# Optimization experiments

Hardware: AMD Instinct MI355X
Metric: run time of the kernel (lower is better)

The kernel has to match this reference:

```python
import jax, jax.numpy as jnp
import numpy as np

B, C, H, W = 8, 256, 64, 64
EPS = 1e-5


def _mk_conv_bn(key, oc, ic):
    k = jax.random.split(key, 6)
    return dict(
        w=jax.random.normal(k[0], (oc, ic), jnp.float32) * 0.01,  # trunc-normal approx, stddev 0.01
        b=jnp.zeros((oc,), jnp.float32),
        s=jax.random.uniform(k[1], (oc,), jnp.float32, 0.5, 1.5),   # BN scale
        t=jax.random.normal(k[2], (oc,), jnp.float32) * 0.1,        # BN shift
        m=jax.random.normal(k[3], (oc,), jnp.float32) * 0.1,        # BN running mean
        v=jax.random.uniform(k[4], (oc,), jnp.float32, 0.5, 1.5),   # BN running var
    )


def setup_inputs() -> dict:
    key = jax.random.key(0)
    ks = jax.random.split(key, 6)
    d = {"x": jax.random.normal(ks[0], (B, C, H, W), jnp.float32)}
    for i, (oc, ic) in zip([1, 2, 3, 4], [(C // 8, C), (C // 8, C), (C // 2, C), (C, C // 2)]):
        p = _mk_conv_bn(ks[i], oc, ic)
        for name, val in p.items():
            d[f"{name}{i}"] = val
    d["gamma"] = jnp.asarray(0.5, jnp.float32)
    return d


def _cbn(x, w, b, s, t, m, v, relu=True):
    # conv1x1 + BatchNorm(eval) [+ ReLU]; dropout is identity at inference
    y = jnp.einsum('bchw,oc->bohw', x, w) + b[None, :, None, None]
    scale = (s / jnp.sqrt(v + EPS))[None, :, None, None]
    y = (y - m[None, :, None, None]) * scale + t[None, :, None, None]
    return jax.nn.relu(y) if relu else y


def _maxpool2(x):
    b, c, h, w = x.shape
    return x.reshape(b, c, h // 2, 2, w // 2, 2).max(axis=(3, 5))


def reference(x, w1, b1, s1, t1, m1, v1, w2, b2, s2, t2, m2, v2,
              w3, b3, s3, t3, m3, v3, w4, b4, s4, t4, m4, v4, gamma):
    b, c, h, w = x.shape
    f = _maxpool2(_cbn(x, w1, b1, s1, t1, m1, v1))   # (B, C/8, H/2, W/2)
    g = _cbn(x, w2, b2, s2, t2, m2, v2)              # (B, C/8, H, W)
    hh = _maxpool2(_cbn(x, w3, b3, s3, t3, m3, v3))  # (B, C/2, H/2, W/2)
    hw, hw4 = h * w, (h // 2) * (w // 2)
    f = f.reshape(b, c // 8, hw4).transpose(0, 2, 1)  # (B, HW/4, C/8)
    g = g.reshape(b, c // 8, hw)                      # (B, C/8, HW)
    s = jnp.einsum('bnk,bkm->bnm', f, g)              # (B, HW/4, HW)
    beta = jax.nn.softmax(s, axis=1)                  # softmax over dim=1, as in source
    hh = hh.reshape(b, c // 2, hw4)                   # (B, C/2, HW/4)
    o = jnp.einsum('bcn,bnm->bcm', hh, beta).reshape(b, c // 2, h, w)
    out = _cbn(o, w4, b4, s4, t4, m4, v4, relu=False)
    return gamma * out + x
```

## Files before the change

kernel.cpp:

```cpp
#include <hip/hip_runtime.h>
#include <hip/hip_bf16.h>

#define HW   4096
#define HW4  1024
#define EPS  1e-5f
#define SM_SHIFT 20.0f

typedef __attribute__((ext_vector_type(8))) short bf16x8;
typedef __attribute__((ext_vector_type(4))) float f32x4;

__device__ __forceinline__ short f2bs(float f) {
    union { float f; unsigned u; } v; v.f = f;
    unsigned r = v.u + 0x7FFFu + ((v.u >> 16) & 1u);
    return (short)(r >> 16);
}
__device__ __forceinline__ float bs2f(short s) {
    union { unsigned u; float f; } v; v.u = ((unsigned)(unsigned short)s) << 16;
    return v.f;
}
__device__ __forceinline__ int swz64(int r, int c)  { return (r << 6) + ((c ^ (r & 7))  << 3); }
__device__ __forceinline__ int swz128(int r, int c) { return (r << 7) + ((c ^ (r & 15)) << 3); }
__device__ __forceinline__ int p40(int r, int c)    { return r * 40 + c * 8; }

__global__ __launch_bounds__(256) void conv123pool(
    const float* __restrict__ x,
    const float* __restrict__ w1, const float* __restrict__ b1, const float* __restrict__ s1,
    const float* __restrict__ t1, const float* __restrict__ m1, const float* __restrict__ v1,
    const float* __restrict__ w2, const float* __restrict__ b2, const float* __restrict__ s2,
    const float* __restrict__ t2, const float* __restrict__ m2, const float* __restrict__ v2,
    const float* __restrict__ w3, const float* __restrict__ b3, const float* __restrict__ s3,
    const float* __restrict__ t3, const float* __restrict__ m3, const float* __restrict__ v3,
    short* __restrict__ gbuf, short* __restrict__ fbuf, short* __restrict__ hhbuf)
{
    __shared__ __align__(16) short Wl[96 * 64];
    __shared__ __align__(16) short Xl[128 * 64];
    __shared__ float alB[96], beB[96];

    const int t = threadIdx.x;
    const int lane = t & 63, wv = t >> 6;
    const int quad = lane >> 4, l16 = lane & 15;
    const int ptile = blockIdx.x;
    const int ocg   = blockIdx.y;
    const int bz    = blockIdx.z;
    const int pBase = ptile * 128;
    const int wcol  = (wv & 1) * 32;
    const int woch  = (wv >> 1) * 48;

    if (t < 96) {
        int j = ocg * 96 + t;
        float pb, ps, ptv, pm, pv;
        if (j < 32)      { pb = b1[j]; ps = s1[j]; ptv = t1[j]; pm = m1[j]; pv = v1[j]; }
        else if (j < 64) { int c = j - 32; pb = b2[c]; ps = s2[c]; ptv = t2[c]; pm = m2[c]; pv = v2[c]; }
        else             { int c = j - 64; pb = b3[c]; ps = s3[c]; ptv = t3[c]; pm = m3[c]; pv = v3[c]; }
        float al = ps * rsqrtf(pv + EPS);
        alB[t] = al; beB[t] = (pb - pm) * al + ptv;
    }

    const f32x4 fzero = {0.f, 0.f, 0.f, 0.f};
    f32x4 acc[3][4];
    #pragma unroll
    for (int i = 0; i < 3; ++i)
        #pragma unroll
        for (int j = 0; j < 4; ++j) acc[i][j] = fzero;

    const int ptOff0 = wcol, ptOff1 = wcol + 16, ptOff2 = wcol + 64, ptOff3 = wcol + 80;
    const int xp  = t & 127, xk8 = t >> 7;

    for (int k0 = 0; k0 < 256; k0 += 64) {
        #pragma unroll
        for (int i = 0; i < 2; ++i) {
            int idx = t + i * 256;
            if (i == 0 || t < 128) {
                int oc = idx >> 2, kb = (idx & 3) * 16;
                int j = ocg * 96 + oc;
                const float* wp = (j < 32) ? (w1 + j * 256)
                                : (j < 64) ? (w2 + (j - 32) * 256)
                                           : (w3 + (j - 64) * 256);
                wp += k0 + kb;
                float4 a = *(const float4*)(wp);
                float4 b = *(const float4*)(wp + 4);
                float4 c = *(const float4*)(wp + 8);
                float4 d = *(const float4*)(wp + 12);
                bf16x8 lo, hi;
                lo[0]=f2bs(a.x); lo[1]=f2bs(a.y); lo[2]=f2bs(a.z); lo[3]=f2bs(a.w);
                lo[4]=f2bs(b.x); lo[5]=f2bs(b.y); lo[6]=f2bs(b.z); lo[7]=f2bs(b.w);
                hi[0]=f2bs(c.x); hi[1]=f2bs(c.y); hi[2]=f2bs(c.z); hi[3]=f2bs(c.w);
                hi[4]=f2bs(d.x); hi[5]=f2bs(d.y); hi[6]=f2bs(d.z); hi[7]=f2bs(d.w);
                *(bf16x8*)&Wl[swz64(oc, (kb >> 3))]     = lo;
                *(bf16x8*)&Wl[swz64(oc, (kb >> 3) + 1)] = hi;
            }
        }
        {
            const float* xp0 = x + ((size_t)bz * 256 + k0 + xk8 * 32) * HW + pBase + xp;
            float fv[32];
            #pragma unroll
            for (int i = 0; i < 32; ++i) fv[i] = xp0[(size_t)i * HW];
            #pragma unroll
            for (int c = 0; c < 4; ++c) {
                bf16x8 v;
                #pragma unroll
                for (int jj = 0; jj < 8; ++jj) v[jj] = f2bs(fv[c * 8 + jj]);
                *(bf16x8*)&Xl[swz64(xp, xk8 * 4 + c)] = v;
            }
        }
        __syncthreads();
        #pragma unroll
        for (int kk = 0; kk < 2; ++kk) {
            bf16x8 bfr[4];
            bfr[0] = *(const bf16x8*)&Xl[swz64(ptOff0 + l16, kk * 4 + quad)];
            bfr[1] = *(const bf16x8*)&Xl[swz64(ptOff1 + l16, kk * 4 + quad)];
            bfr[2] = *(const bf16x8*)&Xl[swz64(ptOff2 + l16, kk * 4 + quad)];
            bfr[3] = *(const bf16x8*)&Xl[swz64(ptOff3 + l16, kk * 4 + quad)];
            #pragma unroll
            for (int tt = 0; tt < 3; ++tt) {
                bf16x8 afr = *(const bf16x8*)&Wl[swz64(woch + tt * 16 + l16, kk * 4 + quad)];
                #pragma unroll
                for (int pt = 0; pt < 4; ++pt)
                    acc[tt][pt] = __builtin_amdgcn_mfma_f32_16x16x32_bf16(afr, bfr[pt], acc[tt][pt], 0, 0, 0);
            }
        }
        __syncthreads();
    }

    #pragma unroll
    for (int tt = 0; tt < 3; ++tt) {
        #pragma unroll
        for (int r = 0; r < 4; ++r) {
            int ocl = woch + tt * 16 + quad * 4 + r;
            int j = ocg * 96 + ocl;
            float al = alB[ocl], be = beB[ocl];
            float y[4];
            y[0] = fmaxf(acc[tt][0][r] * al + be, 0.f);
            y[1] = fmaxf(acc[tt][1][r] * al + be, 0.f);
            y[2] = fmaxf(acc[tt][2][r] * al + be, 0.f);
            y[3] = fmaxf(acc[tt][3][r] * al + be, 0.f);
            if (j >= 32 && j < 64) {
                size_t base = ((size_t)bz * 32 + (j - 32)) * HW + pBase;
                gbuf[base + ptOff0 + l16] = f2bs(y[0]);
                gbuf[base + ptOff1 + l16] = f2bs(y[1]);
                gbuf[base + ptOff2 + l16] = f2bs(y[2]);
                gbuf[base + ptOff3 + l16] = f2bs(y[3]);
            } else {
                #pragma unroll
                for (int c = 0; c < 2; ++c) {
                    float v  = fmaxf(y[c], y[c + 2]);
                    float po = fmaxf(v, __shfl_xor(v, 1));
                    if ((l16 & 1) == 0) {
                        int col = wcol + c * 16 + l16;
                        int n = ptile * 32 + (col >> 1);
                        if (j < 32) fbuf[((size_t)bz * 32 + j) * HW4 + n] = f2bs(po);
                        else        hhbuf[((size_t)bz * 128 + (j - 64)) * HW4 + n] = f2bs(po);
                    }
                }
            }
        }
    }
}

__global__ __launch_bounds__(256, 5) void attn_partial(
    const short* __restrict__ gbuf,
    const short* __restrict__ fbuf,
    const short* __restrict__ hhbuf,
    short* __restrict__ opart,
    float* __restrict__ Zbuf)
{
    __shared__ __align__(16) short smem[13312];
    short* gTl = smem;
    short* fTl = smem + 2560;
    short* sTl = smem + 5120;
    short* hhl = smem + 9216;

    const int t = threadIdx.x;
    const int lane = t & 63, wv = t >> 6;
    const int quad = lane >> 4, l16 = lane & 15;
    const int bz = blockIdx.z;
    const int np = blockIdx.y & 1;
    const int cp = blockIdx.y >> 1;
    const int m0 = blockIdx.x * 64;
    const int ms = wv * 16;
    const f32x4 fzero = {0.f, 0.f, 0.f, 0.f};

    {
        int mm = t & 63, k8 = t >> 6;
        bf16x8 v;
        #pragma unroll
        for (int j = 0; j < 8; ++j)
            v[j] = gbuf[((size_t)bz * 32 + k8 * 8 + j) * HW + m0 + mm];
        *(bf16x8*)&gTl[p40(mm, k8)] = v;
    }
    __syncthreads();
    bf16x8 bg = *(const bf16x8*)&gTl[p40(ms + l16, quad)];

    const int fnn = t & 63, fk8 = t >> 6;
    const int hrow = t >> 3, hnc = t & 7;
    const short* fB = fbuf + (size_t)bz * 32 * HW4;
    const short* hB = hhbuf + ((size_t)bz * 128 + cp * 64) * HW4;

    float psum = 0.f;
    f32x4 oacc[4];
    #pragma unroll
    for (int i = 0; i < 4; ++i) oacc[i] = fzero;

    const int nbase = np * 512;
    for (int n0 = nbase; n0 < nbase + 512; n0 += 64) {
        __syncthreads();
        {
            bf16x8 v;
            #pragma unroll
            for (int j = 0; j < 8; ++j)
                v[j] = fB[(fk8 * 8 + j) * HW4 + n0 + fnn];
            *(bf16x8*)&fTl[p40(fnn, fk8)] = v;
        }
        {
            #pragma unroll
            for (int i = 0; i < 2; ++i)
                *(bf16x8*)&hhl[swz64(i * 32 + hrow, hnc)] =
                    *(const bf16x8*)(hB + (size_t)(i * 32 + hrow) * HW4 + n0 + hnc * 8);
        }
        __syncthreads();

        f32x4 sacc[4];
        #pragma unroll
        for (int nt = 0; nt < 4; ++nt) {
            bf16x8 af = *(const bf16x8*)&fTl[p40(nt * 16 + l16, quad)];
            sacc[nt] = __builtin_amdgcn_mfma_f32_16x16x32_bf16(af, bg, fzero, 0, 0, 0);
        }

        #pragma unroll
        for (int nt = 0; nt < 4; ++nt) {
            short4 ev;
            #pragma unroll
            for (int r = 0; r < 4; ++r) {
                float e = __expf(sacc[nt][r] - SM_SHIFT);
                psum += e;
                ((short*)&ev)[r] = f2bs(e);
            }
            int chunk = nt * 2 + (quad >> 1);
            *(short4*)&sTl[swz64(ms + l16, chunk) + (quad & 1) * 4] = ev;
        }

        #pragma unroll
        for (int kk = 0; kk < 2; ++kk) {
            bf16x8 bs = *(const bf16x8*)&sTl[swz64(ms + l16, kk * 4 + quad)];
            #pragma unroll
            for (int ct = 0; ct < 4; ++ct) {
                bf16x8 ah = *(const bf16x8*)&hhl[swz64(ct * 16 + l16, kk * 4 + quad)];
                oacc[ct] = __builtin_amdgcn_mfma_f32_16x16x32_bf16(ah, bs, oacc[ct], 0, 0, 0);
            }
        }
    }

    psum += __shfl_xor(psum, 16);
    psum += __shfl_xor(psum, 32);
    int m = m0 + ms + l16;
    if (cp == 0 && quad == 0)
        Zbuf[((size_t)bz * 2 + np) * HW + m] = psum;

    #pragma unroll
    for (int ct = 0; ct < 4; ++ct) {
        short4 ov;
        #pragma unroll
        for (int r = 0; r < 4; ++r) ((short*)&ov)[r] = f2bs(oacc[ct][r]);
        *(short4*)(opart + (((size_t)bz * 2 + np) * HW + m) * 128 + cp * 64 + ct * 16 + quad * 4) = ov;
    }
}

__global__ __launch_bounds__(256) void conv4_merge(
    const short* __restrict__ opart,
    const float* __restrict__ Zbuf,
    const float* __restrict__ x,
    const float* __restrict__ w4, const float* __restrict__ b4, const float* __restrict__ s4,
    const float* __restrict__ t4, const float* __restrict__ m4, const float* __restrict__ v4,
    const float* __restrict__ gamma, float* __restrict__ out)
{
    __shared__ __align__(16) short smem[24576];
    __shared__ float alB4[256], beB4[256];
    short* o_l = smem;
    short* Wl4 = smem + 8192;

    const int t = threadIdx.x;
    const int lane = t & 63, wv = t >> 6;
    const int quad = lane >> 4, l16 = lane & 15;
    const int bz = blockIdx.y;
    const int m0 = blockIdx.x * 64;
    const f32x4 fzero = {0.f, 0.f, 0.f, 0.f};

    {
        float al = s4[t] * rsqrtf(v4[t] + EPS);
        alB4[t] = al; beB4[t] = (b4[t] - m4[t]) * al + t4[t];
    }

    {
        int m = t >> 2, cb = (t & 3) * 32;
        size_t mi = (size_t)m0 + m;
        const short* p0 = opart + (((size_t)bz * 2 + 0) * HW + mi) * 128 + cb;
        const short* p1 = opart + (((size_t)bz * 2 + 1) * HW + mi) * 128 + cb;
        float z = Zbuf[((size_t)bz * 2 + 0) * HW + mi] + Zbuf[((size_t)bz * 2 + 1) * HW + mi];
        float inv = 1.0f / z;
        #pragma unroll
        for (int seg = 0; seg < 4; ++seg) {
            bf16x8 a = *(const bf16x8*)(p0 + seg * 8);
            bf16x8 b = *(const bf16x8*)(p1 + seg * 8);
            bf16x8 o;
            #pragma unroll
            for (int j = 0; j < 8; ++j)
                o[j] = f2bs((bs2f(a[j]) + bs2f(b[j])) * inv);
            *(bf16x8*)&o_l[swz128(m, (cb >> 3) + seg)] = o;
        }
    }

    f32x4 acc4[4][4];
    #pragma unroll
    for (int i = 0; i < 4; ++i)
        #pragma unroll
        for (int j = 0; j < 4; ++j) acc4[i][j] = fzero;

    for (int c0 = 0; c0 < 128; c0 += 64) {
        #pragma unroll
        for (int i = 0; i < 4; ++i) {
            int oc = i * 64 + (t >> 2);
            int kb = (t & 3) * 16;
            const float* wp = w4 + oc * 128 + c0 + kb;
            float4 a = *(const float4*)(wp);
            float4 b = *(const float4*)(wp + 4);
            float4 c = *(const float4*)(wp + 8);
            float4 d = *(const float4*)(wp + 12);
            bf16x8 lo, hi;
            lo[0]=f2bs(a.x); lo[1]=f2bs(a.y); lo[2]=f2bs(a.z); lo[3]=f2bs(a.w);
            lo[4]=f2bs(b.x); lo[5]=f2bs(b.y); lo[6]=f2bs(b.z); lo[7]=f2bs(b.w);
            hi[0]=f2bs(c.x); hi[1]=f2bs(c.y); hi[2]=f2bs(c.z); hi[3]=f2bs(c.w);
            hi[4]=f2bs(d.x); hi[5]=f2bs(d.y); hi[6]=f2bs(d.z); hi[7]=f2bs(d.w);
            *(bf16x8*)&Wl4[swz64(oc, (kb >> 3))]     = lo;
            *(bf16x8*)&Wl4[swz64(oc, (kb >> 3) + 1)] = hi;
        }
        __syncthreads();
        #pragma unroll
        for (int kk = 0; kk < 2; ++kk) {
            bf16x8 bfr[4];
            #pragma unroll
            for (int mt = 0; mt < 4; ++mt)
                bfr[mt] = *(const bf16x8*)&o_l[swz128(mt * 16 + l16, (c0 >> 3) + kk * 4 + quad)];
            #pragma unroll
            for (int ot = 0; ot < 4; ++ot) {
                bf16x8 afr = *(const bf16x8*)&Wl4[swz64(wv * 64 + ot * 16 + l16, kk * 4 + quad)];
                #pragma unroll
                for (int mt = 0; mt < 4; ++mt)
                    acc4[ot][mt] = __builtin_amdgcn_mfma_f32_16x16x32_bf16(afr, bfr[mt], acc4[ot][mt], 0, 0, 0);
            }
        }
        __syncthreads();
    }

    float gm = gamma[0];
    #pragma unroll
    for (int ot = 0; ot < 4; ++ot) {
        #pragma unroll
        for (int r = 0; r < 4; ++r) {
            int oc = wv * 64 + ot * 16 + quad * 4 + r;
            float al = alB4[oc], be = beB4[oc];
            #pragma unroll
            for (int mt = 0; mt < 4; ++mt) {
                int p = m0 + mt * 16 + l16;
                float y  = acc4[ot][mt][r] * al + be;
                float xo = x[((size_t)bz * 256 + oc) * HW + p];
                out[((size_t)bz * 256 + oc) * HW + p] = gm * y + xo;
            }
        }
    }
}

extern "C" void kernel_launch(void* const* d_in, const int* in_sizes, int n_in,
                              void* d_out, int out_size, void* d_ws, size_t ws_size,
                              hipStream_t stream)
{
    const float* x  = (const float*)d_in[0];
    const float* w1 = (const float*)d_in[1];
    const float* b1 = (const float*)d_in[2];
    const float* s1 = (const float*)d_in[3];
    const float* t1 = (const float*)d_in[4];
    const float* m1 = (const float*)d_in[5];
    const float* v1 = (const float*)d_in[6];
    const float* w2 = (const float*)d_in[7];
    const float* b2 = (const float*)d_in[8];
    const float* s2 = (const float*)d_in[9];
    const float* t2 = (const float*)d_in[10];
    const float* m2 = (const float*)d_in[11];
    const float* v2 = (const float*)d_in[12];
    const float* w3 = (const float*)d_in[13];
    const float* b3 = (const float*)d_in[14];
    const float* s3 = (const float*)d_in[15];
    const float* t3 = (const float*)d_in[16];
    const float* m3 = (const float*)d_in[17];
    const float* v3 = (const float*)d_in[18];
    const float* w4 = (const float*)d_in[19];
    const float* b4 = (const float*)d_in[20];
    const float* s4 = (const float*)d_in[21];
    const float* t4 = (const float*)d_in[22];
    const float* m4 = (const float*)d_in[23];
    const float* v4 = (const float*)d_in[24];
    const float* gm = (const float*)d_in[25];
    float* out = (float*)d_out;

    short* gbuf  = (short*)d_ws;
    short* fbuf  = gbuf  + (size_t)8 * 32 * 4096;
    short* hhbuf = fbuf  + (size_t)8 * 32 * 1024;
    short* opart = hhbuf + (size_t)8 * 128 * 1024;
    float* Zbuf  = (float*)(opart + (size_t)8 * 2 * 4096 * 128);

    conv123pool<<<dim3(32, 2, 8), 256, 0, stream>>>(
        x, w1, b1, s1, t1, m1, v1, w2, b2, s2, t2, m2, v2, w3, b3, s3, t3, m3, v3,
        gbuf, fbuf, hhbuf);
    attn_partial<<<dim3(64, 4, 8), 256, 0, stream>>>(
        gbuf, fbuf, hhbuf, opart, Zbuf);
    conv4_merge<<<dim3(64, 8), 256, 0, stream>>>(
        opart, Zbuf, x, w4, b4, s4, t4, m4, v4, gm, out);
}
```

Baseline: 179.3 us.

## Fuse attention and conv4 into one kernel, dropping split-N partials

Merges the attention-partial kernel and the conv4 merge kernel into a single kernel. Each block now covers all 1024 keys and all 128 hh channels and normalizes by its own softmax sum. It then runs the conv4 GEMM directly from shared memory, so the bf16 opart and Zbuf round trip through global memory and one launch go away. The trade-off is far less parallelism: 512 blocks instead of 2048, and each block does a longer serial loop with more accumulators, which may lower occupancy and latency hiding.

```diff
diff --git a/kernel.cpp b/kernel.cpp
--- a/kernel.cpp
+++ b/kernel.cpp
@@ -13,10 +13,6 @@
     union { float f; unsigned u; } v; v.f = f;
     unsigned r = v.u + 0x7FFFu + ((v.u >> 16) & 1u);
     return (short)(r >> 16);
-}
-__device__ __forceinline__ float bs2f(short s) {
-    union { unsigned u; float f; } v; v.u = ((unsigned)(unsigned short)s) << 16;
-    return v.f;
 }
 __device__ __forceinline__ int swz64(int r, int c)  { return (r << 6) + ((c ^ (r & 7))  << 3); }
 __device__ __forceinline__ int swz128(int r, int c) { return (r << 7) + ((c ^ (r & 15)) << 3); }
@@ -157,124 +153,21 @@
     }
 }
 
-__global__ __launch_bounds__(256, 5) void attn_partial(
+__global__ __launch_bounds__(256, 4) void attn_conv4(
     const short* __restrict__ gbuf,
     const short* __restrict__ fbuf,
     const short* __restrict__ hhbuf,
-    short* __restrict__ opart,
-    float* __restrict__ Zbuf)
-{
-    __shared__ __align__(16) short smem[13312];
-    short* gTl = smem;
-    short* fTl = smem + 2560;
-    short* sTl = smem + 5120;
-    short* hhl = smem + 9216;
-
-    const int t = threadIdx.x;
-    const int lane = t & 63, wv = t >> 6;
-    const int quad = lane >> 4, l16 = lane & 15;
-    const int bz = blockIdx.z;
-    const int np = blockIdx.y & 1;
-    const int cp = blockIdx.y >> 1;
-    const int m0 = blockIdx.x * 64;
-    const int ms = wv * 16;
-    const f32x4 fzero = {0.f, 0.f, 0.f, 0.f};
-
-    {
-        int mm = t & 63, k8 = t >> 6;
-        bf16x8 v;
-        #pragma unroll
-        for (int j = 0; j < 8; ++j)
-            v[j] = gbuf[((size_t)bz * 32 + k8 * 8 + j) * HW + m0 + mm];
-        *(bf16x8*)&gTl[p40(mm, k8)] = v;
-    }
-    __syncthreads();
-    bf16x8 bg = *(const bf16x8*)&gTl[p40(ms + l16, quad)];
-
-    const int fnn = t & 63, fk8 = t >> 6;
-    const int hrow = t >> 3, hnc = t & 7;
-    const short* fB = fbuf + (size_t)bz * 32 * HW4;
-    const short* hB = hhbuf + ((size_t)bz * 128 + cp * 64) * HW4;
-
-    float psum = 0.f;
-    f32x4 oacc[4];
-    #pragma unroll
-    for (int i = 0; i < 4; ++i) oacc[i] = fzero;
-
-    const int nbase = np * 512;
-    for (int n0 = nbase; n0 < nbase + 512; n0 += 64) {
-        __syncthreads();
-        {
-            bf16x8 v;
-            #pragma unroll
-            for (int j = 0; j < 8; ++j)
-                v[j] = fB[(fk8 * 8 + j) * HW4 + n0 + fnn];
-            *(bf16x8*)&fTl[p40(fnn, fk8)] = v;
-        }
-        {
-            #pragma unroll
-            for (int i = 0; i < 2; ++i)
-                *(bf16x8*)&hhl[swz64(i * 32 + hrow, hnc)] =
-                    *(const bf16x8*)(hB + (size_t)(i * 32 + hrow) * HW4 + n0 + hnc * 8);
-        }
-        __syncthreads();
-
-        f32x4 sacc[4];
-        #pragma unroll
-        for (int nt = 0; nt < 4; ++nt) {
-            bf16x8 af = *(const bf16x8*)&fTl[p40(nt * 16 + l16, quad)];
-            sacc[nt] = __builtin_amdgcn_mfma_f32_16x16x32_bf16(af, bg, fzero, 0, 0, 0);
-        }
-
-        #pragma unroll
-        for (int nt = 0; nt < 4; ++nt) {
-            short4 ev;
-            #pragma unroll
-            for (int r = 0; r < 4; ++r) {
-                float e = __expf(sacc[nt][r] - SM_SHIFT);
-                psum += e;
-                ((short*)&ev)[r] = f2bs(e);
-            }
-            int chunk = nt * 2 + (quad >> 1);
-            *(short4*)&sTl[swz64(ms + l16, chunk) + (quad & 1) * 4] = ev;
-        }
-
-        #pragma unroll
-        for (int kk = 0; kk < 2; ++kk) {
-            bf16x8 bs = *(const bf16x8*)&sTl[swz64(ms + l16, kk * 4 + quad)];
-            #pragma unroll
-            for (int ct = 0; ct < 4; ++ct) {
-                bf16x8 ah = *(const bf16x8*)&hhl[swz64(ct * 16 + l16, kk * 4 + quad)];
-                oacc[ct] = __builtin_amdgcn_mfma_f32_16x16x32_bf16(ah, bs, oacc[ct], 0, 0, 0);
-            }
-        }
-    }
-
-    psum += __shfl_xor(psum, 16);
-    psum += __shfl_xor(psum, 32);
-    int m = m0 + ms + l16;
-    if (cp == 0 && quad == 0)
-        Zbuf[((size_t)bz * 2 + np) * HW + m] = psum;
-
-    #pragma unroll
-    for (int ct = 0; ct < 4; ++ct) {
-        short4 ov;
-        #pragma unroll
-        for (int r = 0; r < 4; ++r) ((short*)&ov)[r] = f2bs(oacc[ct][r]);
-        *(short4*)(opart + (((size_t)bz * 2 + np) * HW + m) * 128 + cp * 64 + ct * 16 + quad * 4) = ov;
-    }
-}
-
-__global__ __launch_bounds__(256) void conv4_merge(
-    const short* __restrict__ opart,
-    const float* __restrict__ Zbuf,
     const float* __restrict__ x,
     const float* __restrict__ w4, const float* __restrict__ b4, const float* __restrict__ s4,
     const float* __restrict__ t4, const float* __restrict__ m4, const float* __restrict__ v4,
     const float* __restrict__ gamma, float* __restrict__ out)
 {
-    __shared__ __align__(16) short smem[24576];
+    __shared__ __align__(16) short smem[18432];
     __shared__ float alB4[256], beB4[256];
+    short* gTl = smem;
+    short* fTl = smem + 2560;
+    short* sTl = smem + 5120;
+    short* hhl = smem + 9216;
     short* o_l = smem;
     short* Wl4 = smem + 8192;
 
@@ -283,6 +176,7 @@
     const int quad = lane >> 4, l16 = lane & 15;
     const int bz = blockIdx.y;
     const int m0 = blockIdx.x * 64;
+    const int ms = wv * 16;
     const f32x4 fzero = {0.f, 0.f, 0.f, 0.f};
 
     {
@@ -291,21 +185,86 @@
     }
 
     {
-        int m = t >> 2, cb = (t & 3) * 32;
-        size_t mi = (size_t)m0 + m;
-        const short* p0 = opart + (((size_t)bz * 2 + 0) * HW + mi) * 128 + cb;
-        const short* p1 = opart + (((size_t)bz * 2 + 1) * HW + mi) * 128 + cb;
-        float z = Zbuf[((size_t)bz * 2 + 0) * HW + mi] + Zbuf[((size_t)bz * 2 + 1) * HW + mi];
-        float inv = 1.0f / z;
-        #pragma unroll
-        for (int seg = 0; seg < 4; ++seg) {
-            bf16x8 a = *(const bf16x8*)(p0 + seg * 8);
-            bf16x8 b = *(const bf16x8*)(p1 + seg * 8);
-            bf16x8 o;
+        int mm = t & 63, k8 = t >> 6;
+        bf16x8 v;
+        #pragma unroll
+        for (int j = 0; j < 8; ++j)
+            v[j] = gbuf[((size_t)bz * 32 + k8 * 8 + j) * HW + m0 + mm];
+        *(bf16x8*)&gTl[p40(mm, k8)] = v;
+    }
+    __syncthreads();
+    bf16x8 bg = *(const bf16x8*)&gTl[p40(ms + l16, quad)];
+
+    const int fnn = t & 63, fk8 = t >> 6;
+    const int hrow = t >> 3, hnc = t & 7;
+    const short* fB = fbuf + (size_t)bz * 32 * HW4;
+    const short* hB = hhbuf + (size_t)bz * 128 * HW4;
+
+    float psum = 0.f;
+    f32x4 oacc[8];
+    #pragma unroll
+    for (int i = 0; i < 8; ++i) oacc[i] = fzero;
+
+    for (int n0 = 0; n0 < 1024; n0 += 64) {
+        __syncthreads();
+        {
+            bf16x8 v;
             #pragma unroll
             for (int j = 0; j < 8; ++j)
-                o[j] = f2bs((bs2f(a[j]) + bs2f(b[j])) * inv);
-            *(bf16x8*)&o_l[swz128(m, (cb >> 3) + seg)] = o;
+                v[j] = fB[(fk8 * 8 + j) * HW4 + n0 + fnn];
+            *(bf16x8*)&fTl[p40(fnn, fk8)] = v;
+        }
+        {
+            #pragma unroll
+            for (int i = 0; i < 4; ++i)
+                *(bf16x8*)&hhl[swz64(i * 32 + hrow, hnc)] =
+                    *(const bf16x8*)(hB + (size_t)(i * 32 + hrow) * HW4 + n0 + hnc * 8);
+        }
+        __syncthreads();
+
+        f32x4 sacc[4];
+        #pragma unroll
+        for (int nt = 0; nt < 4; ++nt) {
+            bf16x8 af = *(const bf16x8*)&fTl[p40(nt * 16 + l16, quad)];
+            sacc[nt] = __builtin_amdgcn_mfma_f32_16x16x32_bf16(af, bg, fzero, 0, 0, 0);
+        }
+
+        #pragma unroll
+        for (int nt = 0; nt < 4; ++nt) {
+            short4 ev;
+            #pragma unroll
+            for (int r = 0; r < 4; ++r) {
+                float e = __expf(sacc[nt][r] - SM_SHIFT);
+                psum += e;
+                ((short*)&ev)[r] = f2bs(e);
+            }
+            int chunk = nt * 2 + (quad >> 1);
+            *(short4*)&sTl[swz64(ms + l16, chunk) + (quad & 1) * 4] = ev;
+        }
+
+        #pragma unroll
+        for (int kk = 0; kk < 2; ++kk) {
+            bf16x8 bs = *(const bf16x8*)&sTl[swz64(ms + l16, kk * 4 + quad)];
+            #pragma unroll
+            for (int ct = 0; ct < 8; ++ct) {
+                bf16x8 ah = *(const bf16x8*)&hhl[swz64(ct * 16 + l16, kk * 4 + quad)];
+                oacc[ct] = __builtin_amdgcn_mfma_f32_16x16x32_bf16(ah, bs, oacc[ct], 0, 0, 0);
+            }
+        }
+    }
+    __syncthreads();
+
+    psum += __shfl_xor(psum, 16);
+    psum += __shfl_xor(psum, 32);
+    {
+        float inv = 1.0f / psum;
+        int m = ms + l16;
+        #pragma unroll
+        for (int ct = 0; ct < 8; ++ct) {
+            short4 ov;
+            #pragma unroll
+            for (int r = 0; r < 4; ++r) ((short*)&ov)[r] = f2bs(oacc[ct][r] * inv);
+            *(short4*)&o_l[swz128(m, ct * 2 + (quad >> 1)) + (quad & 1) * 4] = ov;
         }
     }
 
@@ -315,40 +274,33 @@
         #pragma unroll
         for (int j = 0; j < 4; ++j) acc4[i][j] = fzero;
 
-    for (int c0 = 0; c0 < 128; c0 += 64) {
-        #pragma unroll
-        for (int i = 0; i < 4; ++i) {
-            int oc = i * 64 + (t >> 2);
-            int kb = (t & 3) * 16;
-            const float* wp = w4 + oc * 128 + c0 + kb;
-            float4 a = *(const float4*)(wp);
-            float4 b = *(const float4*)(wp + 4);
-            float4 c = *(const float4*)(wp + 8);
-            float4 d = *(const float4*)(wp + 12);
-            bf16x8 lo, hi;
-            lo[0]=f2bs(a.x); lo[1]=f2bs(a.y); lo[2]=f2bs(a.z); lo[3]=f2bs(a.w);
-            lo[4]=f2bs(b.x); lo[5]=f2bs(b.y); lo[6]=f2bs(b.z); lo[7]=f2bs(b.w);
-            hi[0]=f2bs(c.x); hi[1]=f2bs(c.y); hi[2]=f2bs(c.z); hi[3]=f2bs(c.w);
-            hi[4]=f2bs(d.x); hi[5]=f2bs(d.y); hi[6]=f2bs(d.z); hi[7]=f2bs(d.w);
-            *(bf16x8*)&Wl4[swz64(oc, (kb >> 3))]     = lo;
-            *(bf16x8*)&Wl4[swz64(oc, (kb >> 3) + 1)] = hi;
-        }
-        __syncthreads();
-        #pragma unroll
-        for (int kk = 0; kk < 2; ++kk) {
-            bf16x8 bfr[4];
+    #pragma unroll
+    for (int k0 = 0; k0 < 128; k0 += 32) {
+        __syncthreads();
+        {
+            const float* wp = w4 + t * 128 + k0;
+            #pragma unroll
+            for (int c = 0; c < 4; ++c) {
+                float4 a = *(const float4*)(wp + c * 8);
+                float4 b = *(const float4*)(wp + c * 8 + 4);
+                bf16x8 v;
+                v[0]=f2bs(a.x); v[1]=f2bs(a.y); v[2]=f2bs(a.z); v[3]=f2bs(a.w);
+                v[4]=f2bs(b.x); v[5]=f2bs(b.y); v[6]=f2bs(b.z); v[7]=f2bs(b.w);
+                *(bf16x8*)&Wl4[p40(t, c)] = v;
+            }
+        }
+        __syncthreads();
+        bf16x8 bfr[4];
+        #pragma unroll
+        for (int mt = 0; mt < 4; ++mt)
+            bfr[mt] = *(const bf16x8*)&o_l[swz128(mt * 16 + l16, (k0 >> 3) + quad)];
+        #pragma unroll
+        for (int ot = 0; ot < 4; ++ot) {
+            bf16x8 afr = *(const bf16x8*)&Wl4[p40(wv * 64 + ot * 16 + l16, quad)];
             #pragma unroll
             for (int mt = 0; mt < 4; ++mt)
-                bfr[mt] = *(const bf16x8*)&o_l[swz128(mt * 16 + l16, (c0 >> 3) + kk * 4 + quad)];
-            #pragma unroll
-            for (int ot = 0; ot < 4; ++ot) {
-                bf16x8 afr = *(const bf16x8*)&Wl4[swz64(wv * 64 + ot * 16 + l16, kk * 4 + quad)];
-                #pragma unroll
-                for (int mt = 0; mt < 4; ++mt)
-                    acc4[ot][mt] = __builtin_amdgcn_mfma_f32_16x16x32_bf16(afr, bfr[mt], acc4[ot][mt], 0, 0, 0);
-            }
-        }
-        __syncthreads();
+                acc4[ot][mt] = __builtin_amdgcn_mfma_f32_16x16x32_bf16(afr, bfr[mt], acc4[ot][mt], 0, 0, 0);
+        }
     }
 
     float gm = gamma[0];
@@ -404,14 +356,10 @@
     short* gbuf  = (short*)d_ws;
     short* fbuf  = gbuf  + (size_t)8 * 32 * 4096;
     short* hhbuf = fbuf  + (size_t)8 * 32 * 1024;
-    short* opart = hhbuf + (size_t)8 * 128 * 1024;
-    float* Zbuf  = (float*)(opart + (size_t)8 * 2 * 4096 * 128);
 
     conv123pool<<<dim3(32, 2, 8), 256, 0, stream>>>(
         x, w1, b1, s1, t1, m1, v1, w2, b2, s2, t2, m2, v2, w3, b3, s3, t3, m3, v3,
         gbuf, fbuf, hhbuf);
-    attn_partial<<<dim3(64, 4, 8), 256, 0, stream>>>(
-        gbuf, fbuf, hhbuf, opart, Zbuf);
-    conv4_merge<<<dim3(64, 8), 256, 0, stream>>>(
-        opart, Zbuf, x, w4, b4, s4, t4, m4, v4, gm, out);
+    attn_conv4<<<dim3(64, 8), 256, 0, stream>>>(
+        gbuf, fbuf, hhbuf, x, w4, b4, s4, t4, m4, v4, gm, out);
 }
```

Measured after the change: 172.3 us. 3.9% less time.
